# Kernel tuning notes

Hardware: AMD Instinct MI355X
Metric: run time of the kernel (lower is better)

The kernel has to match this reference:

```python
import jax, jax.numpy as jnp
import numpy as np
from jax import lax

CORR = 16  # corr_size in the original module


def _adaptive_pool16(x):
    # exact adaptive avg pool when H, W divisible by 16 (torch-equivalent)
    B, C, H, W = x.shape
    return x.reshape(B, C, CORR, H // CORR, CORR, W // CORR).mean(axis=(3, 5))


def _l2_normalize(x, eps=1e-12):
    # torch F.normalize default: L2 over dim=1, norm clamped to eps
    n = jnp.sqrt(jnp.sum(x * x, axis=1, keepdims=True))
    return x / jnp.maximum(n, eps)


def _instance_norm(x, eps=1e-5):
    # InstanceNorm2d, affine=False, biased variance over H,W per (b,c)
    mu = x.mean(axis=(2, 3), keepdims=True)
    var = jnp.mean((x - mu) ** 2, axis=(2, 3), keepdims=True)
    return (x - mu) * lax.rsqrt(var + eps)


def _corr_reduce(x, W1, b1, W2, b2):
    # 1x1 conv (256 -> fc) + bias
    y = jnp.einsum('bchw,oc->bohw', x, W1[:, :, 0, 0]) + b1[None, :, None, None]
    y = jax.nn.relu(_instance_norm(y))
    # 3x3 conv, padding=1, stride=1
    y = lax.conv_general_dilated(y, W2, (1, 1), 'SAME',
                                 dimension_numbers=('NCHW', 'OIHW', 'NCHW'))
    return y + b2[None, :, None, None]


def _corr(feat):
    # pooled [B,C,16,16] used as per-sample bank of 256 1x1 conv kernels
    pooled = _adaptive_pool16(feat)                      # [B,C,16,16]
    norm = _l2_normalize(feat)                           # [B,C,H,W]
    B, C = pooled.shape[:2]
    ker = pooled.reshape(B, C, CORR * CORR)              # [B,C,256]
    # corr[b,p,h,w] = sum_c ker[b,c,p] * norm[b,c,h,w]
    return jnp.einsum('bcp,bchw->bphw', ker, norm)


def setup_inputs() -> dict:
    key = jax.random.key(0)
    ks = jax.random.split(key, 6)
    B, C, H, W = 16, 256, 96, 96
    fc = 256
    return {
        'F_infrared': jax.random.normal(ks[0], (B, C, H, W), jnp.float32),
        'F_visible': jax.random.normal(ks[1], (B, C, H, W), jnp.float32),
        'W1': jax.random.normal(ks[2], (fc, CORR * CORR, 1, 1), jnp.float32) * 0.05,
        'b1': jax.random.normal(ks[3], (fc,), jnp.float32) * 0.05,
        'W2': jax.random.normal(ks[4], (fc, fc, 3, 3), jnp.float32) * 0.05,
        'b2': jax.random.normal(ks[5], (fc,), jnp.float32) * 0.05,
    }


def reference(F_infrared, F_visible, W1, b1, W2, b2):
    VIS_corr = _corr_reduce(_corr(F_visible), W1, b1, W2, b2)
    IR_corr = _corr_reduce(_corr(F_infrared), W1, b1, W2, b2)
    return (IR_corr, VIS_corr)
```

## Files before the change

kernel.cpp:

```cpp
#include <hip/hip_runtime.h>
#include <hip/hip_bf16.h>

#define BATCH 16
#define CH    256
#define HH    96
#define WW    96
#define HWSZ  9216
#define FCH   256
#define PP    256

typedef float f32x4 __attribute__((ext_vector_type(4)));
typedef short bf16x8 __attribute__((ext_vector_type(8)));
typedef unsigned short ushortT;

#define APAD_ELEMS 2458624
#define APAD_CHUNKS 307328

__device__ __forceinline__ void gload16(const void* g, void* l) {
    __builtin_amdgcn_global_load_lds((const __attribute__((address_space(1))) void*)g,
                                     (__attribute__((address_space(3))) void*)l, 16, 0, 0);
}
__device__ __forceinline__ float bfu2f(ushortT u) {
    return __uint_as_float(((unsigned)u) << 16);
}
__device__ __forceinline__ ushortT f2bfu(float f) {
    __hip_bfloat16 hb = __float2bfloat16(f);
    return *reinterpret_cast<ushortT*>(&hb);
}

__global__ void fpack_k(const float* __restrict__ feat, ushortT* __restrict__ fpack,
                        float* __restrict__ rnorm)
{
    int b = blockIdx.y;
    int hw = blockIdx.x * 256 + threadIdx.x;
    const float* src = feat + (size_t)b * CH * HWSZ + hw;
    uint4* dst = (uint4*)fpack + (size_t)b * 32 * HWSZ + hw;
    float ss = 0.f;
    for (int cb = 0; cb < 32; ++cb) {
        union { ushortT u[8]; uint4 v; } pk;
#pragma unroll
        for (int i = 0; i < 8; ++i) {
            float v = src[(size_t)(cb * 8 + i) * HWSZ];
            ss += v * v;
            pk.u[i] = f2bfu(v);
        }
        dst[(size_t)cb * HWSZ] = pk.v;
    }
    rnorm[b * HWSZ + hw] = 1.0f / fmaxf(sqrtf(ss), 1e-12f);
}

__global__ void pool16b_k(const ushortT* __restrict__ fpack, float* __restrict__ pooled)
{
    int cb = blockIdx.x, b = blockIdx.y;
    const uint4* fp = (const uint4*)fpack + ((size_t)b * 32 + cb) * HWSZ;
    int t = threadIdx.x;
    int pr = t >> 4, pc = t & 15;
    float s[8] = {};
#pragma unroll
    for (int i = 0; i < 6; ++i) {
#pragma unroll
        for (int j = 0; j < 6; ++j) {
            uint4 v = fp[(pr * 6 + i) * WW + pc * 6 + j];
            const ushortT* u = (const ushortT*)&v;
#pragma unroll
            for (int k = 0; k < 8; ++k) s[k] += bfu2f(u[k]);
        }
    }
#pragma unroll
    for (int k = 0; k < 8; ++k)
        pooled[((size_t)b * CH + cb * 8 + k) * PP + t] = s[k] * (1.0f / 36.0f);
}

__global__ void gemmM_k(const float* __restrict__ W1, const float* __restrict__ pooled,
                        ushortT* __restrict__ Mb16)
{
    int b = blockIdx.z;
    int o0 = blockIdx.y * 16, c0 = blockIdx.x * 16;
    int ty = threadIdx.y, tx = threadIdx.x;
    __shared__ float Ws[16][17], Ps[16][17];
    float acc = 0.f;
    for (int p0 = 0; p0 < PP; p0 += 16) {
        Ws[ty][tx] = W1[(o0 + ty) * PP + p0 + tx];
        Ps[ty][tx] = pooled[((size_t)b * CH + (c0 + ty)) * PP + p0 + tx];
        __syncthreads();
#pragma unroll
        for (int p = 0; p < 16; ++p) acc += Ws[ty][p] * Ps[tx][p];
        __syncthreads();
    }
    int c = c0 + tx, o = o0 + ty;
    Mb16[(((size_t)b * 32 + (c >> 3)) * 256 + o) * 8 + (c & 7)] = f2bfu(acc);
}

__global__ void repack_w2_k(const float* __restrict__ W2, ushortT* __restrict__ W2r2)
{
    int e = blockIdx.x * 256 + threadIdx.x;
    int ci = e & 7, o = (e >> 3) & 255, cb = (e >> 11) & 31, s = e >> 16;
    int c = cb * 8 + ci;
    W2r2[e] = f2bfu(W2[((size_t)o * 256 + c) * 9 + s]);
}

__global__ void zborder_k(uint4* __restrict__ apad)
{
    int bl = blockIdx.x;
    uint4* apC = apad + (size_t)bl * APAD_CHUNKS;
    uint4 z; z.x = 0; z.y = 0; z.z = 0; z.w = 0;
    for (int e = threadIdx.x; e < 3136; e += 256) {
        apC[e] = z;
        apC[(size_t)97 * 32 * 98 + e] = z;
    }
    for (int e = threadIdx.x; e < 3072; e += 256) {
        int row = 1 + (e >> 5), cb = e & 31;
        size_t base = (size_t)(row * 32 + cb) * 98;
        apC[base] = z;
        apC[base + 97] = z;
    }
}

__global__ __launch_bounds__(256, 4) void gemmYm_k(const ushortT* __restrict__ Mb16,
                                                   const ushortT* __restrict__ fpack,
                                                   const float* __restrict__ rnorm,
                                                   ushortT* __restrict__ apad, int b0)
{
    int bl = blockIdx.z, bg = b0 + bl;
    int hw0 = blockIdx.x * 128;
    int o0 = blockIdx.y * 128;
    int tid = threadIdx.x, wave = tid >> 6, lane = tid & 63;
    int wm = wave >> 1, wn = wave & 1;
    int lr = lane & 15, kb = lane >> 4;

    __shared__ __align__(16) char smem[33280];

    const uint4* MbC = (const uint4*)Mb16 + (size_t)bg * 32 * 256;
    const uint4* fpC = (const uint4*)fpack + (size_t)bg * 32 * HWSZ;

    f32x4 acc[4][4] = {};

    auto STAGE = [&](int buf, int s) {
        int cb0 = s * 4;
        uint4* A = (uint4*)smem + (size_t)buf * 1024;
        uint4* B = A + 512;
#pragma unroll
        for (int i = 0; i < 2; ++i) {
            int e = tid + i * 256;
            int kk = e >> 7, j = e & 127;
            gload16(MbC + (size_t)(cb0 + kk) * 256 + o0 + j, A + e);
            gload16(fpC + (size_t)(cb0 + kk) * HWSZ + hw0 + j, B + e);
        }
    };

    STAGE(0, 0);
    for (int s = 0; s < 8; ++s) {
        int buf = s & 1;
        __syncthreads();
        if (s < 7) STAGE(buf ^ 1, s + 1);
        const bf16x8* AsV = (const bf16x8*)(smem + (size_t)buf * 16384);
        const bf16x8* BsV = AsV + 512;
        bf16x8 af[4], bfv[4];
#pragma unroll
        for (int mf = 0; mf < 4; ++mf) af[mf] = AsV[kb * 128 + wm * 64 + mf * 16 + lr];
#pragma unroll
        for (int nf = 0; nf < 4; ++nf) bfv[nf] = BsV[kb * 128 + wn * 64 + nf * 16 + lr];
#pragma unroll
        for (int mf = 0; mf < 4; ++mf)
#pragma unroll
            for (int nf = 0; nf < 4; ++nf)
                acc[mf][nf] = __builtin_amdgcn_mfma_f32_16x16x32_bf16(af[mf], bfv[nf], acc[mf][nf], 0, 0, 0);
    }
    __syncthreads();

    float rn[4];
#pragma unroll
    for (int nf = 0; nf < 4; ++nf)
        rn[nf] = rnorm[(size_t)bg * HWSZ + hw0 + wn * 64 + nf * 16 + lr];

    ushortT* T = (ushortT*)smem;
#pragma unroll
    for (int mf = 0; mf < 4; ++mf)
#pragma unroll
        for (int nf = 0; nf < 4; ++nf)
#pragma unroll
            for (int r = 0; r < 4; ++r)
                T[(wn * 64 + nf * 16 + lr) * 130 + wm * 64 + mf * 16 + kb * 4 + r] =
                    f2bfu(acc[mf][nf][r] * rn[nf]);
    __syncthreads();

    uint4* apC = (uint4*)apad + (size_t)bl * APAD_CHUNKS;
    int ob0 = blockIdx.y * 16;
#pragma unroll
    for (int i = 0; i < 8; ++i) {
        int e = tid + i * 256;
        int hw_l = e >> 4, ob = e & 15;
        uint4 v = *(uint4*)&T[hw_l * 130 + ob * 8];
        int hw = hw0 + hw_l;
        int h = hw / 96, w = hw - h * 96;
        apC[(size_t)((h + 1) * 32 + ob0 + ob) * 98 + (w + 1)] = v;
    }
}

__global__ void instats2_k(const ushortT* __restrict__ apad, float* __restrict__ mu,
                           float* __restrict__ istd)
{
    int ob = blockIdx.x, bl = blockIdx.y;
    const uint4* apC = (const uint4*)apad + (size_t)bl * APAD_CHUNKS;
    float s[8] = {}, s2[8] = {};
    for (int e = threadIdx.x; e < HWSZ; e += 256) {
        int row = e / 96;
        int w = e - row * 96;
        uint4 v = apC[(size_t)((row + 1) * 32 + ob) * 98 + w + 1];
        const ushortT* u = (const ushortT*)&v;
#pragma unroll
        for (int k = 0; k < 8; ++k) {
            float f = bfu2f(u[k]);
            s[k] += f; s2[k] += f * f;
        }
    }
#pragma unroll
    for (int off = 32; off > 0; off >>= 1) {
#pragma unroll
        for (int k = 0; k < 8; ++k) {
            s[k]  += __shfl_down(s[k],  off, 64);
            s2[k] += __shfl_down(s2[k], off, 64);
        }
    }
    __shared__ float sh[4][16];
    int wid = threadIdx.x >> 6;
    if ((threadIdx.x & 63) == 0) {
#pragma unroll
        for (int k = 0; k < 8; ++k) { sh[wid][k] = s[k]; sh[wid][8 + k] = s2[k]; }
    }
    __syncthreads();
    if (threadIdx.x < 8) {
        int k = threadIdx.x;
        float S  = sh[0][k] + sh[1][k] + sh[2][k] + sh[3][k];
        float S2 = sh[0][8 + k] + sh[1][8 + k] + sh[2][8 + k] + sh[3][8 + k];
        float m   = S * (1.0f / HWSZ);
        float var = S2 * (1.0f / HWSZ) - m * m;
        if (var < 0.f) var = 0.f;
        mu[bl * 256 + ob * 8 + k]   = m;
        istd[bl * 256 + ob * 8 + k] = rsqrtf(var + 1e-5f);
    }
}

__global__ void nr_k(ushortT* __restrict__ apad, const float* __restrict__ mu,
                     const float* __restrict__ istd)
{
    int row = blockIdx.x + 1, bl = blockIdx.y;
    __shared__ float smu[256], sis[256];
    smu[threadIdx.x] = mu[bl * 256 + threadIdx.x];
    sis[threadIdx.x] = istd[bl * 256 + threadIdx.x];
    __syncthreads();
    uint4* apC = (uint4*)apad + (size_t)bl * APAD_CHUNKS + (size_t)row * 32 * 98;
    for (int e = threadIdx.x; e < 3072; e += 256) {
        int ob = e / 96;
        int w = e - ob * 96 + 1;
        uint4 v = apC[(size_t)ob * 98 + w];
        ushortT* u = (ushortT*)&v;
#pragma unroll
        for (int k = 0; k < 8; ++k) {
            float f = (bfu2f(u[k]) - smu[ob * 8 + k]) * sis[ob * 8 + k];
            u[k] = f2bfu(f > 0.f ? f : 0.f);
        }
        apC[(size_t)ob * 98 + w] = v;
    }
}

__global__ __launch_bounds__(256, 1) void conv3m5_k(const ushortT* __restrict__ apad,
                                                    const ushortT* __restrict__ W2r2,
                                                    const float* __restrict__ b2,
                                                    float* __restrict__ out)
{
    int h0 = blockIdx.x * 4;
    int o0 = blockIdx.y * 64;
    int bl = blockIdx.z;
    int tid = threadIdx.x;
    int wave = tid >> 6, lane = tid & 63;
    int lr = lane & 15, kb = lane >> 4;

    __shared__ __align__(16) uint4 AsC[2][2304];
    __shared__ __align__(16) uint4 BsC[2][2368];

    const uint4* apadC = (const uint4*)apad + (size_t)bl * APAD_CHUNKS;
    const uint4* w2C   = (const uint4*)W2r2;

    f32x4 acc[4][6] = {};

    auto STAGE = [&](int buf, int ci) {
        int cb0 = ci * 4;
#pragma unroll
        for (int i = 0; i < 9; ++i) {
            int e = tid + i * 256;
            int o = e & 63, kk = (e >> 6) & 3, s = e >> 8;
            gload16(w2C + (size_t)(s * 32 + cb0 + kk) * 256 + o0 + o, &AsC[buf][e]);
        }
#pragma unroll
        for (int i = 0; i < 10; ++i) {
            int e = tid + i * 256;
            if (e < 2352) {
                int w = e % 98, r = e / 98;
                int kk = r & 3, row = r >> 2;
                gload16(apadC + (size_t)((h0 + row) * 32 + cb0 + kk) * 98 + w,
                        &BsC[buf][e]);
            }
        }
    };

    STAGE(0, 0);
    for (int ci = 0; ci < 8; ++ci) {
        int buf = ci & 1;
        __syncthreads();
        if (ci < 7) STAGE(buf ^ 1, ci + 1);
        const bf16x8* AsV = (const bf16x8*)&AsC[buf][0];
        const bf16x8* BsV = (const bf16x8*)&BsC[buf][0];
#pragma unroll
        for (int kh = 0; kh < 3; ++kh) {
#pragma unroll
            for (int kw = 0; kw < 3; ++kw) {
                int s = kh * 3 + kw;
                bf16x8 af[4];
#pragma unroll
                for (int mf = 0; mf < 4; ++mf)
                    af[mf] = AsV[(s * 4 + kb) * 64 + mf * 16 + lr];
#pragma unroll
                for (int nf = 0; nf < 6; ++nf) {
                    bf16x8 bfr = BsV[((wave + kh) * 4 + kb) * 98 + nf * 16 + lr + kw];
#pragma unroll
                    for (int mf = 0; mf < 4; ++mf)
                        acc[mf][nf] = __builtin_amdgcn_mfma_f32_16x16x32_bf16(af[mf], bfr, acc[mf][nf], 0, 0, 0);
                }
            }
        }
    }

    int h = h0 + wave;
    float* obase = out + (size_t)bl * FCH * HWSZ + (size_t)h * WW;
#pragma unroll
    for (int mf = 0; mf < 4; ++mf) {
#pragma unroll
        for (int r = 0; r < 4; ++r) {
            int o = o0 + mf * 16 + kb * 4 + r;
            float bias = b2[o];
            float* orow = obase + (size_t)o * HWSZ;
#pragma unroll
            for (int nf = 0; nf < 6; ++nf)
                orow[nf * 16 + lr] = acc[mf][nf][r] + bias;
        }
    }
}

extern "C" void kernel_launch(void* const* d_in, const int* in_sizes, int n_in,
                              void* d_out, int out_size, void* d_ws, size_t ws_size,
                              hipStream_t stream)
{
    const float* Fir  = (const float*)d_in[0];
    const float* Fvis = (const float*)d_in[1];
    const float* W1   = (const float*)d_in[2];
    const float* W2   = (const float*)d_in[4];
    const float* b2   = (const float*)d_in[5];
    float* out = (float*)d_out;

    char* w = (char*)d_ws;
    const size_t poolB = (size_t)BATCH * CH * PP * 4;
    const size_t MbB   = (size_t)BATCH * 32 * 256 * 8 * 2;
    const size_t rnB   = (size_t)BATCH * HWSZ * 4;
    const size_t stB   = (size_t)BATCH * FCH * 4;
    const size_t w2rB  = (size_t)9 * 32 * 256 * 8 * 2;
    const size_t fpB   = (size_t)BATCH * 32 * HWSZ * 8 * 2;

    size_t off = 0;
    float*   pooled = (float*)(w + off);   off += poolB;
    ushortT* Mb16   = (ushortT*)(w + off); off += MbB;
    float*   rnorm  = (float*)(w + off);   off += rnB;
    float*   mu     = (float*)(w + off);   off += stB;
    float*   istd   = (float*)(w + off);   off += stB;
    ushortT* W2r2   = (ushortT*)(w + off); off += w2rB;
    ushortT* fpack  = (ushortT*)(w + off); off += fpB;
    const size_t fixed = off;

    const size_t apadB = (size_t)APAD_ELEMS * 2;
    size_t avail = ws_size > fixed ? ws_size - fixed : 0;
    int NB = (int)(avail / apadB);
    if (NB > BATCH) NB = BATCH;
    if (NB < 1) NB = 1;
    ushortT* apad = (ushortT*)(w + fixed);

    repack_w2_k<<<2304, 256, 0, stream>>>(W2, W2r2);
    zborder_k<<<NB, 256, 0, stream>>>((uint4*)apad);

    for (int f = 0; f < 2; ++f) {
        const float* feat = (f == 0) ? Fir : Fvis;
        float* o_ = out + (size_t)f * BATCH * FCH * HWSZ;

        fpack_k<<<dim3(36, BATCH), 256, 0, stream>>>(feat, fpack, rnorm);
        pool16b_k<<<dim3(32, BATCH), 256, 0, stream>>>(fpack, pooled);
        gemmM_k<<<dim3(16, 16, BATCH), dim3(16, 16), 0, stream>>>(W1, pooled, Mb16);

        for (int b0 = 0; b0 < BATCH; b0 += NB) {
            int nb = BATCH - b0 < NB ? BATCH - b0 : NB;
            gemmYm_k<<<dim3(72, 2, nb), 256, 0, stream>>>(Mb16, fpack, rnorm, apad, b0);
            instats2_k<<<dim3(32, nb), 256, 0, stream>>>(apad, mu, istd);
            nr_k<<<dim3(96, nb), 256, 0, stream>>>(apad, mu, istd);
            conv3m5_k<<<dim3(24, 4, nb), 256, 0, stream>>>(apad, W2r2, b2,
                                                           o_ + (size_t)b0 * FCH * HWSZ);
        }
    }
}
```

Baseline: 721.8 us.

## Split conv3x3 block into 8 waves and add XCD-aware block swizzle

The 3x3 conv kernel now runs 512 threads per block. Each output row is split between two waves, and each wave computes 48 columns instead of 96, which halves the accumulator registers per wave and doubles the waves available to hide latency. When the full batch of 16 is processed in one launch, an optional swizzle maps linear block IDs so that each XCD handles two batch samples, aiming for better L2 locality of the shared activation rows. Shared-memory A tiles are now read by twice as many waves, so LDS traffic per MFMA goes up.

```diff
diff --git a/kernel.cpp b/kernel.cpp
--- a/kernel.cpp
+++ b/kernel.cpp
@@ -264,16 +264,27 @@
     }
 }
 
-__global__ __launch_bounds__(256, 1) void conv3m5_k(const ushortT* __restrict__ apad,
-                                                    const ushortT* __restrict__ W2r2,
-                                                    const float* __restrict__ b2,
-                                                    float* __restrict__ out)
-{
-    int h0 = blockIdx.x * 4;
-    int o0 = blockIdx.y * 64;
-    int bl = blockIdx.z;
+__global__ __launch_bounds__(512, 1) void conv3m10_k(const ushortT* __restrict__ apad,
+                                                     const ushortT* __restrict__ W2r2,
+                                                     const float* __restrict__ b2,
+                                                     float* __restrict__ out, int swz)
+{
+    int ht, ot, bl;
+    if (swz) {
+        int lin = blockIdx.x + 24 * (blockIdx.y + 4 * blockIdx.z);
+        int xcd = lin & 7, i = lin >> 3;
+        int second = (i >= 96) ? 1 : 0;
+        bl = 2 * xcd + second;
+        int w = i - second * 96;
+        ot = w / 24; ht = w - ot * 24;
+    } else {
+        ht = blockIdx.x; ot = blockIdx.y; bl = blockIdx.z;
+    }
+    int h0 = ht * 4;
+    int o0 = ot * 64;
     int tid = threadIdx.x;
     int wave = tid >> 6, lane = tid & 63;
+    int row = wave >> 1, half = wave & 1;
     int lr = lane & 15, kb = lane >> 4;
 
     __shared__ __align__(16) uint4 AsC[2][2304];
@@ -282,23 +293,26 @@
     const uint4* apadC = (const uint4*)apad + (size_t)bl * APAD_CHUNKS;
     const uint4* w2C   = (const uint4*)W2r2;
 
-    f32x4 acc[4][6] = {};
+    f32x4 acc[4][3] = {};
 
     auto STAGE = [&](int buf, int ci) {
         int cb0 = ci * 4;
 #pragma unroll
-        for (int i = 0; i < 9; ++i) {
-            int e = tid + i * 256;
-            int o = e & 63, kk = (e >> 6) & 3, s = e >> 8;
-            gload16(w2C + (size_t)(s * 32 + cb0 + kk) * 256 + o0 + o, &AsC[buf][e]);
-        }
-#pragma unroll
-        for (int i = 0; i < 10; ++i) {
-            int e = tid + i * 256;
+        for (int i = 0; i < 5; ++i) {
+            int e = tid + i * 512;
+            if (e < 2304) {
+                int o = e & 63, kk = (e >> 6) & 3, s = e >> 8;
+                gload16(w2C + (size_t)(s * 32 + cb0 + kk) * 256 + o0 + o,
+                        &AsC[buf][e]);
+            }
+        }
+#pragma unroll
+        for (int i = 0; i < 5; ++i) {
+            int e = tid + i * 512;
             if (e < 2352) {
                 int w = e % 98, r = e / 98;
-                int kk = r & 3, row = r >> 2;
-                gload16(apadC + (size_t)((h0 + row) * 32 + cb0 + kk) * 98 + w,
+                int kk = r & 3, rr = r >> 2;
+                gload16(apadC + (size_t)((h0 + rr) * 32 + cb0 + kk) * 98 + w,
                         &BsC[buf][e]);
             }
         }
@@ -321,8 +335,9 @@
                 for (int mf = 0; mf < 4; ++mf)
                     af[mf] = AsV[(s * 4 + kb) * 64 + mf * 16 + lr];
 #pragma unroll
-                for (int nf = 0; nf < 6; ++nf) {
-                    bf16x8 bfr = BsV[((wave + kh) * 4 + kb) * 98 + nf * 16 + lr + kw];
+                for (int nf = 0; nf < 3; ++nf) {
+                    bf16x8 bfr = BsV[((row + kh) * 4 + kb) * 98
+                                     + half * 48 + nf * 16 + lr + kw];
 #pragma unroll
                     for (int mf = 0; mf < 4; ++mf)
                         acc[mf][nf] = __builtin_amdgcn_mfma_f32_16x16x32_bf16(af[mf], bfr, acc[mf][nf], 0, 0, 0);
@@ -331,8 +346,8 @@
         }
     }
 
-    int h = h0 + wave;
-    float* obase = out + (size_t)bl * FCH * HWSZ + (size_t)h * WW;
+    int h = h0 + row;
+    float* obase = out + (size_t)bl * FCH * HWSZ + (size_t)h * WW + half * 48;
 #pragma unroll
     for (int mf = 0; mf < 4; ++mf) {
 #pragma unroll
@@ -341,7 +356,7 @@
             float bias = b2[o];
             float* orow = obase + (size_t)o * HWSZ;
 #pragma unroll
-            for (int nf = 0; nf < 6; ++nf)
+            for (int nf = 0; nf < 3; ++nf)
                 orow[nf * 16 + lr] = acc[mf][nf][r] + bias;
         }
     }
@@ -399,8 +414,9 @@
             gemmYm_k<<<dim3(72, 2, nb), 256, 0, stream>>>(Mb16, fpack, rnorm, apad, b0);
             instats2_k<<<dim3(32, nb), 256, 0, stream>>>(apad, mu, istd);
             nr_k<<<dim3(96, nb), 256, 0, stream>>>(apad, mu, istd);
-            conv3m5_k<<<dim3(24, 4, nb), 256, 0, stream>>>(apad, W2r2, b2,
-                                                           o_ + (size_t)b0 * FCH * HWSZ);
-        }
-    }
-}
+            conv3m10_k<<<dim3(24, 4, nb), 512, 0, stream>>>(apad, W2r2, b2,
+                                                            o_ + (size_t)b0 * FCH * HWSZ,
+                                                            nb == 16 ? 1 : 0);
+        }
+    }
+}
```

New measurement: 691.6 us. -4.2%, faster.
